# Kernel tuning notes

Measured on AMD Instinct MI355X. Metric: run time of the kernel, lower is better.

## Reference

```python
import jax, jax.numpy as jnp
import numpy as np

B, T, F_IN, SSL, D, H, L, P, FF = 16, 1024, 1024, 512, 256, 4, 4, 128, 2048
EPS = 1e-5


def layer_norm(x, w, b):
    m = x.mean(-1, keepdims=True)
    v = ((x - m) ** 2).mean(-1, keepdims=True)
    return (x - m) / jnp.sqrt(v + EPS) * w + b


def setup_inputs() -> dict:
    key = jax.random.key(0)
    ks = jax.random.split(key, 16)
    def w(k, shape, s=0.02):
        return jax.random.normal(k, shape, jnp.float32) * s
    inp = {}
    inp["features"] = jax.random.normal(ks[0], (B, T, F_IN), jnp.float32)
    inp["feat_lengths"] = jax.random.randint(ks[1], (B,), T // 2, T + 1)
    inp["phoneme_lengths"] = jax.random.randint(ks[2], (B, P), 1, 17)
    inp["ssl_W"] = w(ks[3], (SSL, F_IN)); inp["ssl_b"] = jnp.zeros((SSL,), jnp.float32)
    inp["ln0_w"] = jnp.ones((SSL,), jnp.float32); inp["ln0_b"] = jnp.zeros((SSL,), jnp.float32)
    inp["conv_W"] = w(ks[4], (D, SSL, 3)); inp["conv_b"] = jnp.zeros((D,), jnp.float32)
    inp["qkv_W"] = w(ks[5], (L, 3 * D, D)); inp["qkv_b"] = jnp.zeros((L, 3 * D), jnp.float32)
    inp["out_W"] = w(ks[6], (L, D, D)); inp["out_b"] = jnp.zeros((L, D), jnp.float32)
    inp["ln1_w"] = jnp.ones((L, D), jnp.float32); inp["ln1_b"] = jnp.zeros((L, D), jnp.float32)
    inp["ff1_W"] = w(ks[7], (L, FF, D)); inp["ff1_b"] = jnp.zeros((L, FF), jnp.float32)
    inp["ff2_W"] = w(ks[8], (L, D, FF)); inp["ff2_b"] = jnp.zeros((L, D), jnp.float32)
    inp["ln2_w"] = jnp.ones((L, D), jnp.float32); inp["ln2_b"] = jnp.zeros((L, D), jnp.float32)
    inp["fs1_W"] = w(ks[9], (D, D)); inp["fs1_b"] = jnp.zeros((D,), jnp.float32)
    inp["fs2_W"] = w(ks[10], (1, D)); inp["fs2_b"] = jnp.zeros((1,), jnp.float32)
    return inp


def reference(features, feat_lengths, phoneme_lengths, ssl_W, ssl_b, ln0_w, ln0_b,
              conv_W, conv_b, qkv_W, qkv_b, out_W, out_b, ln1_w, ln1_b,
              ff1_W, ff1_b, ff2_W, ff2_b, ln2_w, ln2_b, fs1_W, fs1_b, fs2_W, fs2_b):
    # SSL encoder: Linear -> ReLU -> (Dropout eval) -> LayerNorm
    x = jax.nn.relu(features @ ssl_W.T + ssl_b)
    x = layer_norm(x, ln0_w, ln0_b)
    # Conv1d k=3 pad=1 over time, then ReLU
    xc = jnp.transpose(x, (0, 2, 1))  # (B, SSL, T)
    xc = jax.lax.conv_general_dilated(xc, conv_W, (1,), ((1, 1),),
                                      dimension_numbers=("NCH", "OIH", "NCH"))
    xc = xc + conv_b[None, :, None]
    x = jax.nn.relu(jnp.transpose(xc, (0, 2, 1)))  # (B, T, D)

    mask = jnp.arange(T)[None, :] < feat_lengths[:, None]  # (B, T) valid frames
    hd = D // H
    scale = 1.0 / np.sqrt(hd).astype(np.float32)
    # Post-norm TransformerEncoderLayer (PyTorch default), ReLU FFN
    for l in range(L):
        qkv = x @ qkv_W[l].T + qkv_b[l]
        q, k, v = jnp.split(qkv, 3, axis=-1)
        q = q.reshape(B, T, H, hd); k = k.reshape(B, T, H, hd); v = v.reshape(B, T, H, hd)
        s = jnp.einsum("bqhd,bkhd->bhqk", q, k) * scale
        s = jnp.where(mask[:, None, None, :], s, -1e30)
        a = jax.nn.softmax(s, axis=-1)
        o = jnp.einsum("bhqk,bkhd->bqhd", a, v).reshape(B, T, D)
        x = layer_norm(x + o @ out_W[l].T + out_b[l], ln1_w[l], ln1_b[l])
        f = jax.nn.relu(x @ ff1_W[l].T + ff1_b[l]) @ ff2_W[l].T + ff2_b[l]
        x = layer_norm(x + f, ln2_w[l], ln2_b[l])

    fs = jax.nn.relu(x @ fs1_W.T + fs1_b) @ fs2_W.T + fs2_b  # (B, T, 1)
    frame_scores = jnp.where(mask, fs[..., 0], 0.0)

    # Vectorized segment mean (replaces per-element Python loop)
    valid = jnp.cumprod((phoneme_lengths > 0).astype(jnp.int32), axis=1)  # stop at first len<=0
    eff = phoneme_lengths * valid
    cum = jnp.cumsum(eff, axis=1)
    end = jnp.clip(cum, 0, T)
    start = jnp.clip(cum - eff, 0, T)
    cs = jnp.concatenate([jnp.zeros((B, 1), frame_scores.dtype),
                          jnp.cumsum(frame_scores, axis=1)], axis=1)  # (B, T+1)
    seg_sum = jnp.take_along_axis(cs, end, axis=1) - jnp.take_along_axis(cs, start, axis=1)
    cnt = end - start
    phoneme_scores = jnp.where(cnt > 0, seg_sum / jnp.maximum(cnt, 1), 0.0)

    pmask = phoneme_lengths > 0
    psum = (phoneme_scores * pmask).sum(axis=1)
    pcnt = jnp.maximum(pmask.sum(axis=1), 1)
    utterance_score = psum / pcnt
    pstd = jnp.sqrt((((phoneme_scores - utterance_score[:, None]) ** 2) * pmask).sum(axis=1) / pcnt)
    fluency_score = jnp.clip(100.0 - jnp.clip(pstd * 10.0, None, 100.0), 0.0, None)
    prosody_score = 0.5 * (utterance_score + fluency_score)
    return frame_scores, phoneme_scores, utterance_score, fluency_score, prosody_score
```

## Files before the change

kernel.cpp:

```cpp
#include <hip/hip_runtime.h>
#include <math.h>

#define B_   16
#define T_   1024
#define FIN_ 1024
#define SSL_ 512
#define D_   256
#define H_   4
#define HD_  64
#define L_   4
#define P_   128
#define FF_  2048
#define M_   (B_ * T_)
#define LN_EPS 1e-5f

typedef __attribute__((ext_vector_type(8))) short bf16x8;
typedef __attribute__((ext_vector_type(4))) float f32x4;

__device__ inline unsigned short f2bf(float f) {
    unsigned int u = __float_as_uint(f);
    u += 0x7fffu + ((u >> 16) & 1u);
    return (unsigned short)(u >> 16);
}
__device__ inline float bf2f(unsigned short h) {
    return __uint_as_float(((unsigned int)h) << 16);
}
__device__ inline bf16x8 pack8(float4 a, float4 b) {
    bf16x8 t;
    t[0] = (short)f2bf(a.x); t[1] = (short)f2bf(a.y);
    t[2] = (short)f2bf(a.z); t[3] = (short)f2bf(a.w);
    t[4] = (short)f2bf(b.x); t[5] = (short)f2bf(b.y);
    t[6] = (short)f2bf(b.z); t[7] = (short)f2bf(b.w);
    return t;
}
__device__ inline void glds16(const unsigned short* g, unsigned short* l) {
    __builtin_amdgcn_global_load_lds(
        (const __attribute__((address_space(1))) void*)g,
        (__attribute__((address_space(3))) void*)l, 16, 0, 0);
}

__global__ __launch_bounds__(256) void cvt_f2b(
    const float* __restrict__ s, unsigned short* __restrict__ d)
{
    size_t i = ((size_t)blockIdx.x * 256 + threadIdx.x) * 8;
    float4 a = *(const float4*)(s + i);
    float4 b = *(const float4*)(s + i + 4);
    *(bf16x8*)(d + i) = pack8(a, b);
}

__global__ __launch_bounds__(256) void cvt_convw(
    const float* __restrict__ s, unsigned short* __restrict__ d)
{
    int i = blockIdx.x * 256 + threadIdx.x;
    int kk = i >> 17, rem = i & 131071;
    int n = rem >> 9, c = rem & 511;
    d[i] = f2bf(s[(size_t)n * 1536 + c * 3 + kk]);
}

template <int RELU, int OBF>
__global__ __launch_bounds__(256) void gemm_ll(
    const unsigned short* __restrict__ Ab, const unsigned short* __restrict__ Wb,
    const float* __restrict__ bias, void* __restrict__ Cout,
    int Md, int Nd, int Kd)
{
    __shared__ __align__(16) unsigned short As[128 * 32];
    __shared__ __align__(16) unsigned short Bs[128 * 32];
    char* AsB = (char*)As;
    char* BsB = (char*)Bs;

    const int tid = threadIdx.x;
    const int m0 = blockIdx.y * 128, n0 = blockIdx.x * 128;
    const int w = tid >> 6, l = tid & 63;
    const int lr = l & 15, lg = l >> 4;
    const int wr = w >> 1, wc = w & 1;

    f32x4 acc[4][4];
#pragma unroll
    for (int mi = 0; mi < 4; ++mi)
#pragma unroll
        for (int ni = 0; ni < 4; ++ni) acc[mi][ni] = (f32x4){0.f, 0.f, 0.f, 0.f};

    int aoff[4], boff[4];
#pragma unroll
    for (int mi = 0; mi < 4; ++mi) {
        int row = wr * 64 + mi * 16 + lr;
        aoff[mi] = row * 64 + ((lg * 16) ^ (((row >> 1) & 3) << 4));
    }
#pragma unroll
    for (int ni = 0; ni < 4; ++ni) {
        int row = wc * 64 + ni * 16 + lr;
        boff[ni] = row * 64 + ((lg * 16) ^ (((row >> 1) & 3) << 4));
    }
    int srow[2], scp[2];
#pragma unroll
    for (int j = 0; j < 2; ++j) {
        int row = (w * 2 + j) * 16 + (l >> 2);
        srow[j] = row;
        scp[j] = (l & 3) ^ ((row >> 1) & 3);
    }

    for (int k0 = 0; k0 < Kd; k0 += 32) {
        __syncthreads();
#pragma unroll
        for (int j = 0; j < 2; ++j) {
            glds16(Ab + (size_t)(m0 + srow[j]) * Kd + k0 + scp[j] * 8,
                   As + (w * 2 + j) * 512);
            glds16(Wb + (size_t)(n0 + srow[j]) * Kd + k0 + scp[j] * 8,
                   Bs + (w * 2 + j) * 512);
        }
        __syncthreads();
        bf16x8 a[4], bb[4];
#pragma unroll
        for (int mi = 0; mi < 4; ++mi) a[mi] = *(bf16x8*)(AsB + aoff[mi]);
#pragma unroll
        for (int ni = 0; ni < 4; ++ni) bb[ni] = *(bf16x8*)(BsB + boff[ni]);
#pragma unroll
        for (int mi = 0; mi < 4; ++mi)
#pragma unroll
            for (int ni = 0; ni < 4; ++ni)
                acc[mi][ni] = __builtin_amdgcn_mfma_f32_16x16x32_bf16(
                    a[mi], bb[ni], acc[mi][ni], 0, 0, 0);
    }

#pragma unroll
    for (int ni = 0; ni < 4; ++ni) {
        int col = n0 + wc * 64 + ni * 16 + lr;
        float bj = bias[col];
#pragma unroll
        for (int mi = 0; mi < 4; ++mi) {
#pragma unroll
            for (int r = 0; r < 4; ++r) {
                int rowg = m0 + wr * 64 + mi * 16 + lg * 4 + r;
                float v = acc[mi][ni][r] + bj;
                if (RELU) v = fmaxf(v, 0.0f);
                if (OBF) {
                    ((unsigned short*)Cout)[(size_t)rowg * Nd + col] = f2bf(v);
                } else {
                    ((float*)Cout)[(size_t)rowg * Nd + col] = v;
                }
            }
        }
    }
}

__global__ __launch_bounds__(256) void conv_mfma(
    const unsigned short* __restrict__ xb, const unsigned short* __restrict__ wb,
    const float* __restrict__ cb, unsigned short* __restrict__ Xb)
{
    __shared__ __align__(16) unsigned short As[130 * 32];
    __shared__ __align__(16) unsigned short Bs[3 * 128 * 32];
    char* AsB = (char*)As;
    char* BsB = (char*)Bs;

    const int tid = threadIdx.x;
    const int n0 = blockIdx.x * 128, m0 = blockIdx.y * 128;
    const int t0 = m0 & 1023;
    const int w = tid >> 6, l = tid & 63;
    const int lr = l & 15, lg = l >> 4;
    const int wr = w >> 1, wc = w & 1;

    f32x4 acc[4][4];
#pragma unroll
    for (int mi = 0; mi < 4; ++mi)
#pragma unroll
        for (int ni = 0; ni < 4; ++ni) acc[mi][ni] = (f32x4){0.f, 0.f, 0.f, 0.f};

    int aoff[4][3], boff[4][3];
#pragma unroll
    for (int mi = 0; mi < 4; ++mi)
#pragma unroll
        for (int kk = 0; kk < 3; ++kk) {
            int row = wr * 64 + mi * 16 + lr + kk;
            aoff[mi][kk] = row * 64 + ((lg * 16) ^ (((row >> 1) & 3) << 4));
        }
#pragma unroll
    for (int ni = 0; ni < 4; ++ni) {
        int nl = wc * 64 + ni * 16 + lr;
#pragma unroll
        for (int kk = 0; kk < 3; ++kk)
            boff[ni][kk] = kk * 8192 + nl * 64 + ((lg * 16) ^ (((nl >> 1) & 3) << 4));
    }

    for (int c0 = 0; c0 < 512; c0 += 32) {
        __syncthreads();
#pragma unroll
        for (int it = 0; it < 3; ++it) {
            int id = tid + it * 256;
            if (id < 520) {
                int r = id >> 2, ch = id & 3;
                int t = t0 + r - 1;
                bf16x8 v = (bf16x8){0, 0, 0, 0, 0, 0, 0, 0};
                if ((unsigned)t < 1024u)
                    v = *(const bf16x8*)(xb + (size_t)(m0 + r - 1) * 512 + c0 + ch * 8);
                *(bf16x8*)(AsB + r * 64 + ((ch * 16) ^ (((r >> 1) & 3) << 4))) = v;
            }
        }
#pragma unroll
        for (int it = 0; it < 6; ++it) {
            int id = tid + it * 256;
            int kk = id >> 9, rem = id & 511;
            int nl = rem >> 2, ch = rem & 3;
            bf16x8 v = *(const bf16x8*)(wb + (size_t)kk * 131072 +
                                        (size_t)(n0 + nl) * 512 + c0 + ch * 8);
            *(bf16x8*)(BsB + kk * 8192 + nl * 64 +
                       ((ch * 16) ^ (((nl >> 1) & 3) << 4))) = v;
        }
        __syncthreads();
#pragma unroll
        for (int kk = 0; kk < 3; ++kk) {
            bf16x8 bb[4];
#pragma unroll
            for (int ni = 0; ni < 4; ++ni) bb[ni] = *(bf16x8*)(BsB + boff[ni][kk]);
#pragma unroll
            for (int mi = 0; mi < 4; ++mi) {
                bf16x8 a = *(bf16x8*)(AsB + aoff[mi][kk]);
#pragma unroll
                for (int ni = 0; ni < 4; ++ni)
                    acc[mi][ni] = __builtin_amdgcn_mfma_f32_16x16x32_bf16(
                        a, bb[ni], acc[mi][ni], 0, 0, 0);
            }
        }
    }

#pragma unroll
    for (int ni = 0; ni < 4; ++ni) {
        int col = n0 + wc * 64 + ni * 16 + lr;
        float bj = cb[col];
#pragma unroll
        for (int mi = 0; mi < 4; ++mi) {
#pragma unroll
            for (int r = 0; r < 4; ++r) {
                int m = m0 + wr * 64 + mi * 16 + lg * 4 + r;
                float v = fmaxf(acc[mi][ni][r] + bj, 0.0f);
                Xb[(size_t)m * 256 + col] = f2bf(v);
            }
        }
    }
}

__global__ __launch_bounds__(512) void attn_mfma(
    const unsigned short* __restrict__ qkvb, const int* __restrict__ lens,
    unsigned short* __restrict__ Ob)
{
    __shared__ __align__(16) unsigned short Kt[64 * 64];
    __shared__ __align__(16) unsigned short Vt[64 * 64];
    __shared__ __align__(16) unsigned short Pt[8][16 * 64];

    const int qt = blockIdx.x, h = blockIdx.y, b = blockIdx.z;
    const int tid = threadIdx.x;
    const int w = tid >> 6, l = tid & 63;
    const int lr = l & 15, lg = l >> 4;
    const int len = lens[b];
    const int nt = (len + 63) >> 6;
    const size_t base = (size_t)b * (T_ * 768);
    const int q0 = qt * 128 + w * 16;

    char* KtB = (char*)Kt;
    char* VtB = (char*)Vt;
    char* PtB = (char*)(Pt[w]);

    bf16x8 qf[2];
#pragma unroll
    for (int half = 0; half < 2; ++half)
        qf[half] = *(const bf16x8*)(qkvb + base + (size_t)(q0 + lr) * 768 +
                                    h * 64 + lg * 8 + half * 32);

    float mrun = -3e38f, lrun = 0.0f;
    f32x4 acc_o[4];
#pragma unroll
    for (int td = 0; td < 4; ++td) acc_o[td] = (f32x4){0.f, 0.f, 0.f, 0.f};

    const int skr = tid >> 3, skc = tid & 7;

    for (int tk = 0; tk < nt; ++tk) {
        const int kv0 = tk * 64;
        __syncthreads();
        {
            const unsigned short* kp =
                qkvb + base + (size_t)(kv0 + skr) * 768 + h * 64 + 256 + skc * 8;
            *(bf16x8*)(KtB + skr * 128 + ((skc << 4) ^ ((skr & 7) << 4))) =
                *(const bf16x8*)kp;
            bf16x8 vv = *(const bf16x8*)(kp + 256);
#pragma unroll
            for (int j = 0; j < 8; ++j) {
                int d = skc * 8 + j;
                *(unsigned short*)(VtB + d * 128 + ((skr * 2) ^ ((d & 7) << 4))) =
                    (unsigned short)vv[j];
            }
        }
        __syncthreads();

        f32x4 accs[4];
        __builtin_amdgcn_s_setprio(1);
#pragma unroll
        for (int kt = 0; kt < 4; ++kt) {
            int row = kt * 16 + lr;
            int rb = row * 128, sw = (row & 7) << 4;
            bf16x8 k0 = *(bf16x8*)(KtB + rb + ((lg * 16) ^ sw));
            bf16x8 k1 = *(bf16x8*)(KtB + rb + ((lg * 16 + 64) ^ sw));
            f32x4 z = (f32x4){0.f, 0.f, 0.f, 0.f};
            f32x4 t = __builtin_amdgcn_mfma_f32_16x16x32_bf16(k0, qf[0], z, 0, 0, 0);
            accs[kt] = __builtin_amdgcn_mfma_f32_16x16x32_bf16(k1, qf[1], t, 0, 0, 0);
        }
        __builtin_amdgcn_s_setprio(0);

        float p[16];
        float pmax = -3e38f;
#pragma unroll
        for (int kt = 0; kt < 4; ++kt)
#pragma unroll
            for (int r = 0; r < 4; ++r) {
                int kidx = kv0 + kt * 16 + lg * 4 + r;
                float v = (kidx < len) ? accs[kt][r] * 0.125f : -1e30f;
                p[kt * 4 + r] = v;
                pmax = fmaxf(pmax, v);
            }
        pmax = fmaxf(pmax, __shfl_xor(pmax, 16));
        pmax = fmaxf(pmax, __shfl_xor(pmax, 32));
        float mnew = fmaxf(mrun, pmax);
        float alpha = __expf(mrun - mnew);
        float psum = 0.0f;
#pragma unroll
        for (int i = 0; i < 16; ++i) {
            float e = __expf(p[i] - mnew);
            p[i] = e;
            psum += e;
        }
        psum += __shfl_xor(psum, 16);
        psum += __shfl_xor(psum, 32);
        lrun = lrun * alpha + psum;
        mrun = mnew;
#pragma unroll
        for (int td = 0; td < 4; ++td) acc_o[td] *= alpha;

        const int swq = (lr & 7) << 4;
#pragma unroll
        for (int kt = 0; kt < 4; ++kt) {
            unsigned int p01 = (unsigned int)f2bf(p[kt * 4 + 0]) |
                               ((unsigned int)f2bf(p[kt * 4 + 1]) << 16);
            unsigned int p23 = (unsigned int)f2bf(p[kt * 4 + 2]) |
                               ((unsigned int)f2bf(p[kt * 4 + 3]) << 16);
            uint2 pw; pw.x = p01; pw.y = p23;
            *(uint2*)(PtB + lr * 128 + ((kt * 32 + lg * 8) ^ swq)) = pw;
        }
        bf16x8 pf0 = *(bf16x8*)(PtB + lr * 128 + ((lg * 16) ^ swq));
        bf16x8 pf1 = *(bf16x8*)(PtB + lr * 128 + ((lg * 16 + 64) ^ swq));
        __builtin_amdgcn_s_setprio(1);
#pragma unroll
        for (int td = 0; td < 4; ++td) {
            int d = td * 16 + lr;
            int db = d * 128, swd = (d & 7) << 4;
            bf16x8 v0 = *(bf16x8*)(VtB + db + ((lg * 16) ^ swd));
            bf16x8 v1 = *(bf16x8*)(VtB + db + ((lg * 16 + 64) ^ swd));
            acc_o[td] = __builtin_amdgcn_mfma_f32_16x16x32_bf16(v0, pf0, acc_o[td], 0, 0, 0);
            acc_o[td] = __builtin_amdgcn_mfma_f32_16x16x32_bf16(v1, pf1, acc_o[td], 0, 0, 0);
        }
        __builtin_amdgcn_s_setprio(0);
    }

    float inv = 1.0f / lrun;
    const int tglob = q0 + lr;
#pragma unroll
    for (int td = 0; td < 4; ++td)
#pragma unroll
        for (int r = 0; r < 4; ++r) {
            int d = td * 16 + lg * 4 + r;
            Ob[((size_t)b * T_ + tglob) * 256 + h * 64 + d] = f2bf(acc_o[td][r] * inv);
        }
}

__global__ __launch_bounds__(256) void ln0_bf16(
    const unsigned short* __restrict__ xin, const float* __restrict__ w,
    const float* __restrict__ b, unsigned short* __restrict__ out)
{
    const int lane = threadIdx.x & 63;
    const int wv = threadIdx.x >> 6;
    const int row = blockIdx.x * 4 + wv;

    bf16x8 v8 = *(const bf16x8*)(xin + (size_t)row * 512 + lane * 8);
    float f[8];
    float s = 0.0f, sq = 0.0f;
#pragma unroll
    for (int j = 0; j < 8; ++j) {
        f[j] = bf2f((unsigned short)v8[j]);
        s += f[j];
        sq += f[j] * f[j];
    }
#pragma unroll
    for (int d = 1; d < 64; d <<= 1) {
        s += __shfl_xor(s, d);
        sq += __shfl_xor(sq, d);
    }
    float mean = s / 512.0f;
    float var = fmaxf(sq / 512.0f - mean * mean, 0.0f);
    float inv = 1.0f / sqrtf(var + LN_EPS);
    float4 w0 = *(const float4*)(w + lane * 8);
    float4 w1 = *(const float4*)(w + lane * 8 + 4);
    float4 b0 = *(const float4*)(b + lane * 8);
    float4 b1 = *(const float4*)(b + lane * 8 + 4);
    float wv8[8] = {w0.x, w0.y, w0.z, w0.w, w1.x, w1.y, w1.z, w1.w};
    float bv8[8] = {b0.x, b0.y, b0.z, b0.w, b1.x, b1.y, b1.z, b1.w};
    bf16x8 o;
#pragma unroll
    for (int j = 0; j < 8; ++j)
        o[j] = (short)f2bf((f[j] - mean) * inv * wv8[j] + bv8[j]);
    *(bf16x8*)(out + (size_t)row * 512 + lane * 8) = o;
}

__global__ __launch_bounds__(256) void ln_res_bf16(
    const unsigned short* __restrict__ t1, const unsigned short* __restrict__ resid,
    const float* __restrict__ w, const float* __restrict__ b,
    unsigned short* __restrict__ out)
{
    const int lane = threadIdx.x & 63;
    const int wv = threadIdx.x >> 6;
    const int row = blockIdx.x * 4 + wv;
    const size_t off = (size_t)row * 256 + lane * 4;

    uint2 a2 = *(const uint2*)(t1 + off);
    uint2 r2 = *(const uint2*)(resid + off);
    float t[4];
    t[0] = bf2f((unsigned short)(a2.x & 0xffff)) + bf2f((unsigned short)(r2.x & 0xffff));
    t[1] = bf2f((unsigned short)(a2.x >> 16))   + bf2f((unsigned short)(r2.x >> 16));
    t[2] = bf2f((unsigned short)(a2.y & 0xffff)) + bf2f((unsigned short)(r2.y & 0xffff));
    t[3] = bf2f((unsigned short)(a2.y >> 16))   + bf2f((unsigned short)(r2.y >> 16));

    float s = t[0] + t[1] + t[2] + t[3];
    float sq = t[0] * t[0] + t[1] * t[1] + t[2] * t[2] + t[3] * t[3];
#pragma unroll
    for (int d = 1; d < 64; d <<= 1) {
        s += __shfl_xor(s, d);
        sq += __shfl_xor(sq, d);
    }
    float mean = s / 256.0f;
    float var = fmaxf(sq / 256.0f - mean * mean, 0.0f);
    float inv = 1.0f / sqrtf(var + LN_EPS);
    float4 wc = *(const float4*)(w + lane * 4);
    float4 bc = *(const float4*)(b + lane * 4);
    float o0 = (t[0] - mean) * inv * wc.x + bc.x;
    float o1 = (t[1] - mean) * inv * wc.y + bc.y;
    float o2 = (t[2] - mean) * inv * wc.z + bc.z;
    float o3 = (t[3] - mean) * inv * wc.w + bc.w;
    uint2 ob;
    ob.x = (unsigned int)f2bf(o0) | ((unsigned int)f2bf(o1) << 16);
    ob.y = (unsigned int)f2bf(o2) | ((unsigned int)f2bf(o3) << 16);
    *(uint2*)(out + off) = ob;
}

__global__ __launch_bounds__(256) void frame_score_kernel(
    const unsigned short* __restrict__ hbuf, const float* __restrict__ w2,
    const float* __restrict__ b2, const int* __restrict__ lens,
    float* __restrict__ frame_out)
{
    const int lane = threadIdx.x & 63;
    const int wv = threadIdx.x >> 6;
    const int rowm = blockIdx.x * 4 + wv;
    uint2 h2 = *(const uint2*)(hbuf + (size_t)rowm * 256 + lane * 4);
    float4 w4 = *(const float4*)(w2 + lane * 4);
    float s = bf2f((unsigned short)(h2.x & 0xffff)) * w4.x +
              bf2f((unsigned short)(h2.x >> 16)) * w4.y +
              bf2f((unsigned short)(h2.y & 0xffff)) * w4.z +
              bf2f((unsigned short)(h2.y >> 16)) * w4.w;
#pragma unroll
    for (int d = 1; d < 64; d <<= 1) s += __shfl_xor(s, d);
    if (lane == 0) {
        int b = rowm >> 10, t = rowm & 1023;
        float fs = s + b2[0];
        frame_out[rowm] = (t < lens[b]) ? fs : 0.0f;
    }
}

__global__ __launch_bounds__(64) void phoneme_kernel(
    const float* __restrict__ frame, const int* __restrict__ plen,
    float* __restrict__ pscore, float* __restrict__ utt,
    float* __restrict__ flu, float* __restrict__ pros)
{
    __shared__ float cs[T_ + 1];
    __shared__ float ps[P_];
    __shared__ int pmk[P_];

    const int b = blockIdx.x;
    const int lane = threadIdx.x;

    float loc[16];
    float run = 0.0f;
#pragma unroll
    for (int i = 0; i < 16; ++i) {
        run += frame[(size_t)b * T_ + lane * 16 + i];
        loc[i] = run;
    }
    float lanesum = run;
    float incl = lanesum;
#pragma unroll
    for (int d = 1; d < 64; d <<= 1) {
        float y = __shfl_up(incl, d);
        if (lane >= d) incl += y;
    }
    float excl = incl - lanesum;
#pragma unroll
    for (int i = 0; i < 16; ++i) cs[lane * 16 + i + 1] = loc[i] + excl;
    if (lane == 0) cs[0] = 0.0f;
    __syncthreads();

    if (lane == 0) {
        int cum = 0, valid = 1;
        float psum = 0.0f;
        int pcnt = 0;
        for (int p = 0; p < P_; ++p) {
            int lp = plen[b * P_ + p];
            if (lp <= 0) valid = 0;
            int eff = valid ? lp : 0;
            int start = cum; if (start > T_) start = T_; if (start < 0) start = 0;
            cum += eff;
            int end = cum; if (end > T_) end = T_; if (end < 0) end = 0;
            int cnt = end - start;
            float score = (cnt > 0) ? (cs[end] - cs[start]) / (float)cnt : 0.0f;
            ps[p] = score;
            pmk[p] = (lp > 0) ? 1 : 0;
            if (lp > 0) { psum += score; pcnt += 1; }
            pscore[b * P_ + p] = score;
        }
        int pc = pcnt > 0 ? pcnt : 1;
        float u = psum / (float)pc;
        float vsum = 0.0f;
        for (int p = 0; p < P_; ++p) {
            float d = ps[p] - u;
            if (pmk[p]) vsum += d * d;
        }
        float pstd = sqrtf(vsum / (float)pc);
        float f = 100.0f - fminf(pstd * 10.0f, 100.0f);
        f = fmaxf(f, 0.0f);
        utt[b] = u;
        flu[b] = f;
        pros[b] = 0.5f * (u + f);
    }
}

extern "C" void kernel_launch(void* const* d_in, const int* in_sizes, int n_in,
                              void* d_out, int out_size, void* d_ws, size_t ws_size,
                              hipStream_t stream)
{
    const float* features = (const float*)d_in[0];
    const int* feat_len = (const int*)d_in[1];
    const int* plen = (const int*)d_in[2];
    const float* ssl_W = (const float*)d_in[3];
    const float* ssl_b = (const float*)d_in[4];
    const float* ln0_w = (const float*)d_in[5];
    const float* ln0_b = (const float*)d_in[6];
    const float* conv_W = (const float*)d_in[7];
    const float* conv_b = (const float*)d_in[8];
    const float* qkv_W = (const float*)d_in[9];
    const float* qkv_b = (const float*)d_in[10];
    const float* out_W = (const float*)d_in[11];
    const float* out_b = (const float*)d_in[12];
    const float* ln1_w = (const float*)d_in[13];
    const float* ln1_b = (const float*)d_in[14];
    const float* ff1_W = (const float*)d_in[15];
    const float* ff1_b = (const float*)d_in[16];
    const float* ff2_W = (const float*)d_in[17];
    const float* ff2_b = (const float*)d_in[18];
    const float* ln2_w = (const float*)d_in[19];
    const float* ln2_b = (const float*)d_in[20];
    const float* fs1_W = (const float*)d_in[21];
    const float* fs1_b = (const float*)d_in[22];
    const float* fs2_W = (const float*)d_in[23];
    const float* fs2_b = (const float*)d_in[24];

    char* base = (char*)d_ws;
    unsigned short* FFb = (unsigned short*)base;
    unsigned short* featb = FFb;
    unsigned short* QKVb = (unsigned short*)(base + (size_t)M_ * 2048 * 2);
    unsigned short* x512b = QKVb;
    unsigned short* Xb = (unsigned short*)((char*)QKVb + (size_t)M_ * 768 * 2);
    unsigned short* Ob = Xb + (size_t)M_ * 256;
    unsigned short* T1b = Ob + (size_t)M_ * 256;
    unsigned short* sslWb = T1b + (size_t)M_ * 256;
    unsigned short* convWb = sslWb + 512 * 1024;
    unsigned short* qkvWb = convWb + 3 * 256 * 512;
    unsigned short* outWb = qkvWb + (size_t)L_ * 768 * 256;
    unsigned short* ff1Wb = outWb + (size_t)L_ * 256 * 256;
    unsigned short* ff2Wb = ff1Wb + (size_t)L_ * 2048 * 256;
    unsigned short* fs1Wb = ff2Wb + (size_t)L_ * 256 * 2048;

    float* frame = (float*)d_out;
    float* pscore = frame + M_;
    float* uttp = pscore + B_ * P_;
    float* flup = uttp + B_;
    float* prosp = flup + B_;

    cvt_f2b<<<8192, 256, 0, stream>>>(features, featb);
    cvt_f2b<<<256, 256, 0, stream>>>(ssl_W, sslWb);
    cvt_convw<<<1536, 256, 0, stream>>>(conv_W, convWb);
    cvt_f2b<<<384, 256, 0, stream>>>(qkv_W, qkvWb);
    cvt_f2b<<<128, 256, 0, stream>>>(out_W, outWb);
    cvt_f2b<<<1024, 256, 0, stream>>>(ff1_W, ff1Wb);
    cvt_f2b<<<1024, 256, 0, stream>>>(ff2_W, ff2Wb);
    cvt_f2b<<<32, 256, 0, stream>>>(fs1_W, fs1Wb);

    gemm_ll<1, 1><<<dim3(SSL_ / 128, M_ / 128), 256, 0, stream>>>(
        featb, sslWb, ssl_b, x512b, M_, SSL_, FIN_);
    ln0_bf16<<<M_ / 4, 256, 0, stream>>>(x512b, ln0_w, ln0_b, x512b);

    conv_mfma<<<dim3(2, M_ / 128), 256, 0, stream>>>(x512b, convWb, conv_b, Xb);

    for (int l = 0; l < L_; ++l) {
        gemm_ll<0, 1><<<dim3(768 / 128, M_ / 128), 256, 0, stream>>>(
            Xb, qkvWb + (size_t)l * 768 * 256, qkv_b + l * 768, QKVb, M_, 768, 256);
        attn_mfma<<<dim3(8, H_, B_), 512, 0, stream>>>(QKVb, feat_len, Ob);
        gemm_ll<0, 1><<<dim3(256 / 128, M_ / 128), 256, 0, stream>>>(
            Ob, outWb + (size_t)l * 256 * 256, out_b + l * 256, T1b, M_, 256, 256);
        ln_res_bf16<<<M_ / 4, 256, 0, stream>>>(
            T1b, Xb, ln1_w + l * 256, ln1_b + l * 256, Xb);
        gemm_ll<1, 1><<<dim3(FF_ / 128, M_ / 128), 256, 0, stream>>>(
            Xb, ff1Wb + (size_t)l * FF_ * 256, ff1_b + l * FF_, FFb, M_, FF_, 256);
        gemm_ll<0, 1><<<dim3(256 / 128, M_ / 128), 256, 0, stream>>>(
            FFb, ff2Wb + (size_t)l * 256 * FF_, ff2_b + l * 256, T1b, M_, 256, FF_);
        ln_res_bf16<<<M_ / 4, 256, 0, stream>>>(
            T1b, Xb, ln2_w + l * 256, ln2_b + l * 256, Xb);
    }

    gemm_ll<1, 1><<<dim3(256 / 128, M_ / 128), 256, 0, stream>>>(
        Xb, fs1Wb, fs1_b, T1b, M_, 256, 256);
    frame_score_kernel<<<M_ / 4, 256, 0, stream>>>(T1b, fs2_W, fs2_b, feat_len, frame);

    phoneme_kernel<<<B_, 64, 0, stream>>>(frame, plen, pscore, uttp, flup, prosp);
}
```

Baseline: 933.6 us.

## Prefetch next K/V tile into registers and add lazy softmax rescaling in attention

```diff
diff --git a/kernel.cpp b/kernel.cpp
--- a/kernel.cpp
+++ b/kernel.cpp
@@ -271,24 +271,44 @@
     for (int td = 0; td < 4; ++td) acc_o[td] = (f32x4){0.f, 0.f, 0.f, 0.f};
 
     const int skr = tid >> 3, skc = tid & 7;
+    const int kOff = skr * 128 + ((skc << 4) ^ ((skr & 7) << 4));
+    const unsigned short* kSrc = qkvb + base + h * 64 + 256 +
+                                 (size_t)skr * 768 + skc * 8;
+    const int vkp = tid >> 4, vdq = tid & 15;
+    const int d0 = vdq * 4;
+    const int vO0 = (d0 + 0) * 128 + ((4 * vkp) ^ (((d0 + 0) & 7) << 4));
+    const int vO1 = (d0 + 1) * 128 + ((4 * vkp) ^ (((d0 + 1) & 7) << 4));
+    const int vO2 = (d0 + 2) * 128 + ((4 * vkp) ^ (((d0 + 2) & 7) << 4));
+    const int vO3 = (d0 + 3) * 128 + ((4 * vkp) ^ (((d0 + 3) & 7) << 4));
+    const unsigned short* vSrcA = qkvb + base + h * 64 + 512 +
+                                  (size_t)(2 * vkp) * 768 + d0;
+    const unsigned short* vSrcB = vSrcA + 768;
+
+    bf16x8 kreg = *(const bf16x8*)kSrc;
+    uint2 va = *(const uint2*)vSrcA;
+    uint2 vb = *(const uint2*)vSrcB;
 
     for (int tk = 0; tk < nt; ++tk) {
         const int kv0 = tk * 64;
         __syncthreads();
+        *(bf16x8*)(KtB + kOff) = kreg;
         {
-            const unsigned short* kp =
-                qkvb + base + (size_t)(kv0 + skr) * 768 + h * 64 + 256 + skc * 8;
-            *(bf16x8*)(KtB + skr * 128 + ((skc << 4) ^ ((skr & 7) << 4))) =
-                *(const bf16x8*)kp;
-            bf16x8 vv = *(const bf16x8*)(kp + 256);
-#pragma unroll
-            for (int j = 0; j < 8; ++j) {
-                int d = skc * 8 + j;
-                *(unsigned short*)(VtB + d * 128 + ((skr * 2) ^ ((d & 7) << 4))) =
-                    (unsigned short)vv[j];
-            }
+            unsigned int w0 = (va.x & 0xffffu) | (vb.x << 16);
+            unsigned int w1 = (va.x >> 16) | (vb.x & 0xffff0000u);
+            unsigned int w2 = (va.y & 0xffffu) | (vb.y << 16);
+            unsigned int w3 = (va.y >> 16) | (vb.y & 0xffff0000u);
+            *(unsigned int*)(VtB + vO0) = w0;
+            *(unsigned int*)(VtB + vO1) = w1;
+            *(unsigned int*)(VtB + vO2) = w2;
+            *(unsigned int*)(VtB + vO3) = w3;
         }
         __syncthreads();
+        if (tk + 1 < nt) {
+            size_t nb = (size_t)(tk + 1) * 64 * 768;
+            kreg = *(const bf16x8*)(kSrc + nb);
+            va = *(const uint2*)(vSrcA + nb);
+            vb = *(const uint2*)(vSrcB + nb);
+        }
 
         f32x4 accs[4];
         __builtin_amdgcn_s_setprio(1);
@@ -306,32 +326,45 @@
 
         float p[16];
         float pmax = -3e38f;
-#pragma unroll
-        for (int kt = 0; kt < 4; ++kt)
-#pragma unroll
-            for (int r = 0; r < 4; ++r) {
-                int kidx = kv0 + kt * 16 + lg * 4 + r;
-                float v = (kidx < len) ? accs[kt][r] * 0.125f : -1e30f;
-                p[kt * 4 + r] = v;
+        if (kv0 + 64 <= len) {
+#pragma unroll
+            for (int i = 0; i < 16; ++i) {
+                float v = accs[i >> 2][i & 3] * 0.125f;
+                p[i] = v;
                 pmax = fmaxf(pmax, v);
             }
+        } else {
+#pragma unroll
+            for (int kt = 0; kt < 4; ++kt)
+#pragma unroll
+                for (int r = 0; r < 4; ++r) {
+                    int kidx = kv0 + kt * 16 + lg * 4 + r;
+                    float v = (kidx < len) ? accs[kt][r] * 0.125f : -1e30f;
+                    p[kt * 4 + r] = v;
+                    pmax = fmaxf(pmax, v);
+                }
+        }
         pmax = fmaxf(pmax, __shfl_xor(pmax, 16));
         pmax = fmaxf(pmax, __shfl_xor(pmax, 32));
-        float mnew = fmaxf(mrun, pmax);
-        float alpha = __expf(mrun - mnew);
+
+        float alpha = 1.0f;
+        if (!__all((int)(pmax <= mrun + 8.0f))) {
+            float mnew = fmaxf(mrun, pmax);
+            alpha = __expf(mrun - mnew);
+            mrun = mnew;
+#pragma unroll
+            for (int td = 0; td < 4; ++td) acc_o[td] *= alpha;
+        }
         float psum = 0.0f;
 #pragma unroll
         for (int i = 0; i < 16; ++i) {
-            float e = __expf(p[i] - mnew);
+            float e = __expf(p[i] - mrun);
             p[i] = e;
             psum += e;
         }
         psum += __shfl_xor(psum, 16);
         psum += __shfl_xor(psum, 32);
         lrun = lrun * alpha + psum;
-        mrun = mnew;
-#pragma unroll
-        for (int td = 0; td < 4; ++td) acc_o[td] *= alpha;
 
         const int swq = (lr & 7) << 4;
 #pragma unroll
```

New measurement: 900.8 us. 1.04x faster.
